# Optimization experiments

Hardware: AMD Instinct MI355X
Metric: run time of the kernel (lower is better)

The kernel has to match this reference:

```python
import jax, jax.numpy as jnp
import numpy as np

B, S, D = 2, 2048, 1024
H, DK, DV = 16, 64, 64


def setup_inputs() -> dict:
    key = jax.random.key(0)
    ks = jax.random.split(key, 9)
    s = 0.02
    return {
        "x": jax.random.normal(ks[0], (B, S, D), dtype=jnp.float32),
        "mask": jnp.zeros((B, S), dtype=bool),  # True = padded position
        "Wq": jax.random.normal(ks[1], (D, H * DK), dtype=jnp.float32) * s,
        "bq": jnp.zeros((H * DK,), dtype=jnp.float32),
        "Wk": jax.random.normal(ks[2], (D, H * DK), dtype=jnp.float32) * s,
        "bk": jnp.zeros((H * DK,), dtype=jnp.float32),
        "Wv": jax.random.normal(ks[3], (D, H * DV), dtype=jnp.float32) * s,
        "bv": jnp.zeros((H * DV,), dtype=jnp.float32),
        "Wo": jax.random.normal(ks[4], (H * DV, D), dtype=jnp.float32) * s,
        "bo": jnp.zeros((D,), dtype=jnp.float32),
    }


def reference(x, mask, Wq, bq, Wk, bk, Wv, bv, Wo, bo):
    Bx, Sx, _ = x.shape
    # projections -> [B, H, S, dk/dv]
    q = (x @ Wq + bq).reshape(Bx, Sx, H, DK).transpose(0, 2, 1, 3)
    k = (x @ Wk + bk).reshape(Bx, Sx, H, DK).transpose(0, 2, 1, 3)
    v = (x @ Wv + bv).reshape(Bx, Sx, H, DV).transpose(0, 2, 1, 3)
    # scaled QK^T: [B, H, Sq, Sk]
    scores = jnp.einsum("bhqd,bhkd->bhqk", q, k) / jnp.sqrt(jnp.float32(DK))
    neg_inf = jnp.float32(-jnp.inf)
    # padding mask: True masks out key positions
    scores = jnp.where(mask[:, None, None, :], neg_inf, scores)
    # causal mask
    causal = jnp.triu(jnp.ones((Sx, Sx), dtype=bool), k=1)
    scores = jnp.where(causal[None, None, :, :], neg_inf, scores)
    attn = jax.nn.softmax(scores, axis=-1)
    out = jnp.einsum("bhqk,bhkd->bhqd", attn, v)  # [B, H, S, dv]
    out = out.transpose(0, 2, 1, 3).reshape(Bx, Sx, H * DV)
    return out @ Wo + bo
```

## Files before the change

kernel.cpp:

```cpp
#include <hip/hip_runtime.h>
#include <stdint.h>

typedef __bf16 bf16_t;
typedef __bf16 bf16x8 __attribute__((ext_vector_type(8)));
typedef float f32x4 __attribute__((ext_vector_type(4)));

#define S_LEN 2048
#define D_MODEL 1024
#define NH 16
#define DKV 64
#define BATCH 2

#define QSCALE 0.1803368801111204f

__device__ __forceinline__ uint16_t f2bfu(float f) {
    union { float f; uint32_t u; } c; c.f = f;
    return (uint16_t)((c.u + 0x7fffu + ((c.u >> 16) & 1u)) >> 16);
}
__device__ __forceinline__ bf16_t f2bf(float f) {
    union { uint16_t s; bf16_t b; } o; o.s = f2bfu(f);
    return o.b;
}
__device__ __forceinline__ uint32_t pack2t(float lo, float hi) {
    union { float f; uint32_t u; } a, b; a.f = lo; b.f = hi;
    return __builtin_amdgcn_perm(b.u, a.u, 0x07060302);
}
__device__ __forceinline__ uint32_t pack2r(float lo, float hi) {
    union { float f; uint32_t u; } a, b; a.f = lo; b.f = hi;
    uint32_t alo = a.u + 0x7fffu + ((a.u >> 16) & 1u);
    uint32_t bhi = b.u + 0x7fffu + ((b.u >> 16) & 1u);
    return __builtin_amdgcn_perm(bhi, alo, 0x07060302);
}
__device__ __forceinline__ float exp2_native(float x) {
    float r;
    asm("v_exp_f32 %0, %1" : "=v"(r) : "v"(x));
    return r;
}
__device__ __forceinline__ void gld_lds16(const bf16_t* g, bf16_t* l) {
    __builtin_amdgcn_global_load_lds(
        (const __attribute__((address_space(1))) void*)g,
        (__attribute__((address_space(3))) void*)l, 16, 0, 0);
}

__global__ __launch_bounds__(256) void k_prep(
    const float* __restrict__ x, bf16_t* __restrict__ xb,
    const float* __restrict__ Wq, const float* __restrict__ Wk,
    const float* __restrict__ Wv, const float* __restrict__ Wo,
    bf16_t* __restrict__ WqkvT, bf16_t* __restrict__ WoT) {
    __shared__ float tile[64][65];
    int bid = blockIdx.x;
    if (bid < 4096) {
        int i = (bid * 256 + threadIdx.x) * 4;
        float4 v = *(const float4*)(x + i);
        xb[i + 0] = f2bf(v.x);
        xb[i + 1] = f2bf(v.y);
        xb[i + 2] = f2bf(v.z);
        xb[i + 3] = f2bf(v.w);
        return;
    }
    int b2 = bid - 4096;
    int k0 = (b2 & 15) * 64;
    int n0 = (b2 >> 4) * 64;
    const float* W; bf16_t* WT; int np, nw;
    if (n0 < 3072) {
        W = (n0 < 1024) ? Wq : (n0 < 2048) ? Wk : Wv;
        np = n0 & 1023; WT = WqkvT; nw = n0;
    } else {
        W = Wo; np = n0 - 3072; WT = WoT; nw = n0 - 3072;
    }
    int tx = threadIdx.x & 63, ty = threadIdx.x >> 6;
    #pragma unroll
    for (int r = ty; r < 64; r += 4)
        tile[r][tx] = W[(size_t)(k0 + r) * 1024 + np + tx];
    __syncthreads();
    #pragma unroll
    for (int r = ty; r < 64; r += 4)
        WT[(size_t)(nw + r) * 1024 + k0 + tx] = f2bf(tile[tx][r]);
}

#define BM 128
#define BN 128
#define BKK 64

__global__ __launch_bounds__(256) void k_gemm_qkv(
    const bf16_t* __restrict__ A, const bf16_t* __restrict__ BT, int K,
    const float* __restrict__ bias0, const float* __restrict__ bias1,
    const float* __restrict__ bias2,
    bf16_t* __restrict__ outQ, bf16_t* __restrict__ outK, bf16_t* __restrict__ outVt) {
    __shared__ __align__(16) bf16_t smem[BM * BKK + BN * BKK];
    bf16_t* const As = smem;
    bf16_t* const Bs = smem + BM * BKK;
    int m0 = blockIdx.x * BM;
    int n0 = blockIdx.y * BN;
    int t = threadIdx.x;
    int wid = t >> 6, lane = t & 63, l15 = lane & 15, quad = lane >> 4;
    int wr = (wid >> 1) * 64, wc = (wid & 1) * 64;
    int srow = t >> 3;
    int schunk = (t & 7) ^ (srow & 7);
    int sldst = (t & 7) * 8;
    const f32x4 fzero = {0.f, 0.f, 0.f, 0.f};
    f32x4 acc[4][4];
    #pragma unroll
    for (int i = 0; i < 4; i++)
        #pragma unroll
        for (int j = 0; j < 4; j++) acc[i][j] = fzero;

    int secb = n0 >> 10;
    int r7 = l15 & 7;
    for (int k0 = 0; k0 < K; k0 += BKK) {
        #pragma unroll
        for (int p = 0; p < 4; p++) {
            int r = p * 32 + srow;
            gld_lds16(&A[(size_t)(m0 + r) * K + k0 + schunk * 8], &As[r * 64 + sldst]);
            gld_lds16(&BT[(size_t)(n0 + r) * K + k0 + schunk * 8], &Bs[r * 64 + sldst]);
        }
        __syncthreads();
        if (secb == 2) {
            #pragma unroll
            for (int kk = 0; kk < BKK; kk += 32) {
                int g = quad + (kk >> 3);
                int col = ((g ^ r7) << 3);
                bf16x8 af[4], bfr[4];
                #pragma unroll
                for (int mt = 0; mt < 4; mt++)
                    af[mt] = *(const bf16x8*)&As[(wr + mt * 16 + l15) * 64 + col];
                #pragma unroll
                for (int nt = 0; nt < 4; nt++)
                    bfr[nt] = *(const bf16x8*)&Bs[(wc + nt * 16 + l15) * 64 + col];
                #pragma unroll
                for (int mt = 0; mt < 4; mt++)
                    #pragma unroll
                    for (int nt = 0; nt < 4; nt++)
                        acc[mt][nt] = __builtin_amdgcn_mfma_f32_16x16x32_bf16(
                            af[mt], bfr[nt], acc[mt][nt], 0, 0, 0);
            }
        } else {
            #pragma unroll
            for (int kk = 0; kk < BKK; kk += 32) {
                int g = quad + (kk >> 3);
                int col = ((g ^ r7) << 3);
                bf16x8 af[4], bfr[4];
                #pragma unroll
                for (int mt = 0; mt < 4; mt++)
                    af[mt] = *(const bf16x8*)&As[(wr + mt * 16 + l15) * 64 + col];
                #pragma unroll
                for (int nt = 0; nt < 4; nt++)
                    bfr[nt] = *(const bf16x8*)&Bs[(wc + nt * 16 + l15) * 64 + col];
                #pragma unroll
                for (int i = 0; i < 4; i++)
                    #pragma unroll
                    for (int j = 0; j < 4; j++)
                        acc[i][j] = __builtin_amdgcn_mfma_f32_16x16x32_bf16(
                            bfr[i], af[j], acc[i][j], 0, 0, 0);
            }
        }
        __syncthreads();
    }

    if (secb == 2) {
        bf16_t* const Ct = smem;
        int nbase = n0 & 1023;
        #pragma unroll
        for (int mt = 0; mt < 4; mt++) {
            #pragma unroll
            for (int nt = 0; nt < 4; nt++) {
                int dl = wc + nt * 16 + l15;
                float bv = bias2[nbase + dl];
                int sl = wr + mt * 16 + quad * 4;
                uint2 pk;
                pk.x = pack2t(acc[mt][nt][0] + bv, acc[mt][nt][1] + bv);
                pk.y = pack2t(acc[mt][nt][2] + bv, acc[mt][nt][3] + bv);
                int c4 = (sl >> 2) ^ ((dl & 7) << 1);
                *(uint2*)&Ct[dl * 128 + c4 * 4] = pk;
            }
        }
        __syncthreads();
        int b = m0 >> 11, sb = m0 & 2047;
        #pragma unroll
        for (int rr = 0; rr < 8; rr++) {
            int row = rr * 16 + (t >> 4);
            int s8 = t & 15;
            int c4 = (s8 * 2) ^ ((row & 7) << 1);
            uint4 vv = *(const uint4*)&Ct[row * 128 + c4 * 4];
            int nn = nbase + row;
            int h = nn >> 6, d = nn & 63;
            *(uint4*)&outVt[(((size_t)(b * NH + h)) * DKV + d) * S_LEN + sb + s8 * 8] = vv;
        }
        return;
    }

    {
        const float* bias = (secb == 0) ? bias0 : bias1;
        bf16_t* outP = (secb == 0) ? outQ : outK;
        float scale = (secb == 0) ? QSCALE : 1.0f;
        #pragma unroll
        for (int i = 0; i < 4; i++) {
            #pragma unroll
            for (int j = 0; j < 4; j++) {
                int nn = (n0 + wc + i * 16 + quad * 4) & 1023;
                float4 bv = *(const float4*)&bias[nn];
                int gr = m0 + wr + j * 16 + l15;
                int b = gr >> 11, s = gr & 2047;
                int h = nn >> 6, d0 = nn & 63;
                float v0 = (acc[i][j][0] + bv.x) * scale;
                float v1 = (acc[i][j][1] + bv.y) * scale;
                float v2 = (acc[i][j][2] + bv.z) * scale;
                float v3 = (acc[i][j][3] + bv.w) * scale;
                uint2 pk;
                pk.x = pack2r(v0, v1);
                pk.y = pack2r(v2, v3);
                *(uint2*)&outP[(((size_t)(b * NH + h)) * S_LEN + s) * DKV + d0] = pk;
            }
        }
    }
}

__global__ __launch_bounds__(256) void k_gemm_out(
    const bf16_t* __restrict__ A, const bf16_t* __restrict__ BT, int N, int K,
    const float* __restrict__ bias, float* __restrict__ outF) {
    __shared__ __align__(16) bf16_t As[128 * 64];
    __shared__ __align__(16) bf16_t Bs[64 * 64];
    int m0 = blockIdx.x * 128;
    int n0 = blockIdx.y * 64;
    int t = threadIdx.x;
    int wid = t >> 6, lane = t & 63, l15 = lane & 15, quad = lane >> 4;
    int wr = wid * 32;
    int srow = t >> 3;
    int schunk = (t & 7) ^ (srow & 7);
    int sldst = (t & 7) * 8;
    const f32x4 fzero = {0.f, 0.f, 0.f, 0.f};
    f32x4 acc[4][2];
    #pragma unroll
    for (int i = 0; i < 4; i++)
        #pragma unroll
        for (int j = 0; j < 2; j++) acc[i][j] = fzero;

    int r7 = l15 & 7;
    for (int k0 = 0; k0 < K; k0 += 64) {
        #pragma unroll
        for (int p = 0; p < 4; p++) {
            int r = p * 32 + srow;
            gld_lds16(&A[(size_t)(m0 + r) * K + k0 + schunk * 8], &As[r * 64 + sldst]);
        }
        #pragma unroll
        for (int p = 0; p < 2; p++) {
            int r = p * 32 + srow;
            gld_lds16(&BT[(size_t)(n0 + r) * K + k0 + schunk * 8], &Bs[r * 64 + sldst]);
        }
        __syncthreads();
        #pragma unroll
        for (int kk = 0; kk < 64; kk += 32) {
            int g = quad + (kk >> 3);
            int col = ((g ^ r7) << 3);
            bf16x8 af[2], bfr[4];
            #pragma unroll
            for (int j = 0; j < 2; j++)
                af[j] = *(const bf16x8*)&As[(wr + j * 16 + l15) * 64 + col];
            #pragma unroll
            for (int i = 0; i < 4; i++)
                bfr[i] = *(const bf16x8*)&Bs[(i * 16 + l15) * 64 + col];
            #pragma unroll
            for (int i = 0; i < 4; i++)
                #pragma unroll
                for (int j = 0; j < 2; j++)
                    acc[i][j] = __builtin_amdgcn_mfma_f32_16x16x32_bf16(
                        bfr[i], af[j], acc[i][j], 0, 0, 0);
        }
        __syncthreads();
    }

    #pragma unroll
    for (int i = 0; i < 4; i++) {
        #pragma unroll
        for (int j = 0; j < 2; j++) {
            int nc = n0 + i * 16 + quad * 4;
            float4 bv = *(const float4*)&bias[nc];
            int mr = m0 + wr + j * 16 + l15;
            float4 o;
            o.x = acc[i][j][0] + bv.x;
            o.y = acc[i][j][1] + bv.y;
            o.z = acc[i][j][2] + bv.z;
            o.w = acc[i][j][3] + bv.w;
            *(float4*)&outF[(size_t)mr * N + nc] = o;
        }
    }
}

__global__ __launch_bounds__(256, 4) void k_attn11(
    const bf16_t* __restrict__ Q, const bf16_t* __restrict__ Kg,
    const bf16_t* __restrict__ Vt, const unsigned char* __restrict__ mask,
    bf16_t* __restrict__ O) {
    __shared__ __align__(16) bf16_t Ks0[64 * 64];
    __shared__ __align__(16) bf16_t Ks1[64 * 64];
    __shared__ __align__(16) bf16_t Vs0[64 * 64];
    __shared__ __align__(16) bf16_t Vs1[64 * 64];
    __shared__ __align__(16) bf16_t Ps[64 * 64];

    int bid = blockIdx.x;
    int bh = bid & 31;
    int u = bid >> 5;
    int a = u & 7, g2 = u >> 3;
    int qt = (g2 == 0) ? 31 - a : (g2 == 1) ? a : (g2 == 2) ? 23 - a : 8 + a;
    int b = bh >> 4, h = bh & 15;
    int t = threadIdx.x;
    int w = t >> 6, lane = t & 63, l15 = lane & 15, quad = lane >> 4;
    int r7 = l15 & 7;

    bool maskany;
    {
        const uint2* mrow = (const uint2*)&mask[b * S_LEN];
        uint2 m0 = mrow[lane], m1 = mrow[lane + 64];
        uint2 m2 = mrow[lane + 128], m3 = mrow[lane + 192];
        uint32_t mo = (m0.x | m0.y) | (m1.x | m1.y) | (m2.x | m2.y) | (m3.x | m3.y);
        maskany = __any(mo != 0);
    }

    const bf16_t* Qrow = Q + ((size_t)bh * S_LEN + qt * 64 + w * 16 + l15) * DKV;
    bf16x8 qf0 = *(const bf16x8*)&Qrow[quad * 8];
    bf16x8 qf1 = *(const bf16x8*)&Qrow[32 + quad * 8];

    const bf16_t* Kbh = Kg + (size_t)bh * S_LEN * DKV;
    const bf16_t* Vbh = Vt + (size_t)bh * DKV * S_LEN;

    const f32x4 fzero = {0.f, 0.f, 0.f, 0.f};
    f32x4 oacc[4];
    f32x4 lacc = fzero;
    #pragma unroll
    for (int nt = 0; nt < 4; nt++) oacc[nt] = fzero;

    const bf16_t one_b = (bf16_t)1.0f;
    const bf16x8 onesf = {one_b, one_b, one_b, one_b, one_b, one_b, one_b, one_b};

    int qg = qt * 64 + w * 16 + l15;

    int sr = t >> 3;
    int sc = (t & 7) ^ (sr & 7);
    int sl = (t & 7) * 8;

    #pragma unroll
    for (int p = 0; p < 2; p++) {
        int r = p * 32 + sr;
        gld_lds16(&Kbh[(size_t)r * DKV + sc * 8], &Ks0[r * 64 + sl]);
        gld_lds16(&Vbh[(size_t)r * S_LEN + sc * 8], &Vs0[r * 64 + sl]);
    }
    __syncthreads();

    auto TILE = [&](const bf16_t* __restrict__ Kr, const bf16_t* __restrict__ Vr,
                    bf16_t* __restrict__ Kw, bf16_t* __restrict__ Vw, int kt) {
        if (kt < qt) {
            int kb2 = (kt + 1) * 64;
            #pragma unroll
            for (int p = 0; p < 2; p++) {
                int r = p * 32 + sr;
                gld_lds16(&Kbh[(size_t)(kb2 + r) * DKV + sc * 8], &Kw[r * 64 + sl]);
                gld_lds16(&Vbh[(size_t)r * S_LEN + kb2 + sc * 8], &Vw[r * 64 + sl]);
            }
        }
        int kbase = kt * 64;

        f32x4 sacc[4];
        #pragma unroll
        for (int mt = 0; mt < 4; mt++) sacc[mt] = fzero;
        #pragma unroll
        for (int kk = 0; kk < 64; kk += 32) {
            bf16x8 qf = kk ? qf1 : qf0;
            int col = (((quad + (kk >> 3)) ^ r7) << 3);
            bf16x8 af[4];
            #pragma unroll
            for (int mt = 0; mt < 4; mt++)
                af[mt] = *(const bf16x8*)&Kr[(mt * 16 + l15) * 64 + col];
            __builtin_amdgcn_s_setprio(1);
            #pragma unroll
            for (int mt = 0; mt < 4; mt++)
                sacc[mt] = __builtin_amdgcn_mfma_f32_16x16x32_bf16(af[mt], qf, sacc[mt], 0, 0, 0);
            __builtin_amdgcn_s_setprio(0);
        }

        if (maskany) {
            #pragma unroll
            for (int mt = 0; mt < 4; mt++) {
                uint32_t mb = *(const uint32_t*)&mask[b * S_LEN + kbase + mt * 16 + quad * 4];
                #pragma unroll
                for (int r = 0; r < 4; r++)
                    sacc[mt][r] += (float)((mb >> (8 * r)) & 0xffu) * -1e30f;
            }
        }
        if (kt == qt) {
            #pragma unroll
            for (int mt = 0; mt < 4; mt++) {
                int kgb = kbase + mt * 16 + quad * 4;
                #pragma unroll
                for (int r = 0; r < 4; r++)
                    if (kgb + r > qg) sacc[mt][r] = -1e30f;
            }
        }
        #pragma unroll
        for (int mt = 0; mt < 4; mt++) {
            uint2 pk;
            pk.x = pack2t(exp2_native(sacc[mt][0]), exp2_native(sacc[mt][1]));
            pk.y = pack2t(exp2_native(sacc[mt][2]), exp2_native(sacc[mt][3]));
            int pc = (mt * 2 + (quad >> 1)) ^ r7;
            *(uint2*)&Ps[(w * 16 + l15) * 64 + pc * 8 + (quad & 1) * 4] = pk;
        }

        #pragma unroll
        for (int kk = 0; kk < 64; kk += 32) {
            bf16x8 pf = *(const bf16x8*)&Ps[(w * 16 + l15) * 64 +
                                             (((quad + (kk >> 3)) ^ r7) << 3)];
            int vcol = (((quad + (kk >> 3)) ^ r7) << 3);
            bf16x8 vf[4];
            #pragma unroll
            for (int nt = 0; nt < 4; nt++)
                vf[nt] = *(const bf16x8*)&Vr[(nt * 16 + l15) * 64 + vcol];
            __builtin_amdgcn_s_setprio(1);
            #pragma unroll
            for (int nt = 0; nt < 4; nt++)
                oacc[nt] = __builtin_amdgcn_mfma_f32_16x16x32_bf16(pf, vf[nt], oacc[nt], 0, 0, 0);
            lacc = __builtin_amdgcn_mfma_f32_16x16x32_bf16(pf, onesf, lacc, 0, 0, 0);
            __builtin_amdgcn_s_setprio(0);
        }

        if (kt < qt) __syncthreads();
    };

    for (int kt = 0; kt <= qt; kt += 2) {
        TILE(Ks0, Vs0, Ks1, Vs1, kt);
        if (kt + 1 <= qt) TILE(Ks1, Vs1, Ks0, Vs0, kt + 1);
    }

    #pragma unroll
    for (int r = 0; r < 4; r++) {
        float l = lacc[r];
        float invl = l > 0.f ? 1.f / l : 0.f;
        int q = qt * 64 + w * 16 + quad * 4 + r;
        #pragma unroll
        for (int nt = 0; nt < 4; nt++) {
            int d = nt * 16 + l15;
            O[((size_t)b * S_LEN + q) * D_MODEL + h * DKV + d] = f2bf(oacc[nt][r] * invl);
        }
    }
}

extern "C" void kernel_launch(void* const* d_in, const int* in_sizes, int n_in,
                              void* d_out, int out_size, void* d_ws, size_t ws_size,
                              hipStream_t stream) {
    const float* x = (const float*)d_in[0];
    const unsigned char* mask = (const unsigned char*)d_in[1];
    const float* Wq = (const float*)d_in[2];
    const float* bq = (const float*)d_in[3];
    const float* Wk = (const float*)d_in[4];
    const float* bk = (const float*)d_in[5];
    const float* Wv = (const float*)d_in[6];
    const float* bv = (const float*)d_in[7];
    const float* Wo = (const float*)d_in[8];
    const float* bo = (const float*)d_in[9];
    float* out = (float*)d_out;

    char* ws = (char*)d_ws;
    const size_t MB = 1024 * 1024;
    bf16_t* xb    = (bf16_t*)(ws + 0 * MB);
    bf16_t* WqkvT = (bf16_t*)(ws + 8 * MB);
    bf16_t* WoT   = (bf16_t*)(ws + 14 * MB);
    bf16_t* Qb    = (bf16_t*)(ws + 16 * MB);
    bf16_t* Kb    = (bf16_t*)(ws + 24 * MB);
    bf16_t* Vtb   = (bf16_t*)(ws + 32 * MB);
    bf16_t* AOb   = (bf16_t*)(ws + 40 * MB);

    k_prep<<<dim3(4096 + 1024), dim3(256), 0, stream>>>(
        x, xb, Wq, Wk, Wv, Wo, WqkvT, WoT);
    k_gemm_qkv<<<dim3(32, 24), dim3(256), 0, stream>>>(
        xb, WqkvT, 1024, bq, bk, bv, Qb, Kb, Vtb);
    k_attn11<<<dim3(1024), dim3(256), 0, stream>>>(Qb, Kb, Vtb, mask, AOb);
    k_gemm_out<<<dim3(32, 16), dim3(256), 0, stream>>>(
        AOb, WoT, 1024, 1024, bo, out);
}
```

Measured before the change: 181.3 us.

## Double query tile per block to reuse K/V tiles across two row groups

After: 194.3 us. 7.2% more time.

```diff
diff --git a/kernel.cpp b/kernel.cpp
--- a/kernel.cpp
+++ b/kernel.cpp
@@ -286,7 +286,7 @@
     }
 }
 
-__global__ __launch_bounds__(256, 4) void k_attn11(
+__global__ __launch_bounds__(256, 2) void k_attn12(
     const bf16_t* __restrict__ Q, const bf16_t* __restrict__ Kg,
     const bf16_t* __restrict__ Vt, const unsigned char* __restrict__ mask,
     bf16_t* __restrict__ O) {
@@ -294,13 +294,12 @@
     __shared__ __align__(16) bf16_t Ks1[64 * 64];
     __shared__ __align__(16) bf16_t Vs0[64 * 64];
     __shared__ __align__(16) bf16_t Vs1[64 * 64];
-    __shared__ __align__(16) bf16_t Ps[64 * 64];
+    __shared__ __align__(16) bf16_t Ps[128 * 64];
 
     int bid = blockIdx.x;
     int bh = bid & 31;
     int u = bid >> 5;
-    int a = u & 7, g2 = u >> 3;
-    int qt = (g2 == 0) ? 31 - a : (g2 == 1) ? a : (g2 == 2) ? 23 - a : 8 + a;
+    int qt = (u < 8) ? (15 - u) : (u - 8);
     int b = bh >> 4, h = bh & 15;
     int t = threadIdx.x;
     int w = t >> 6, lane = t & 63, l15 = lane & 15, quad = lane >> 4;
@@ -315,23 +314,28 @@
         maskany = __any(mo != 0);
     }
 
-    const bf16_t* Qrow = Q + ((size_t)bh * S_LEN + qt * 64 + w * 16 + l15) * DKV;
-    bf16x8 qf0 = *(const bf16x8*)&Qrow[quad * 8];
-    bf16x8 qf1 = *(const bf16x8*)&Qrow[32 + quad * 8];
+    const bf16_t* Q0 = Q + ((size_t)bh * S_LEN + qt * 128 + w * 32 + l15) * DKV;
+    bf16x8 qf[2][2];
+    qf[0][0] = *(const bf16x8*)&Q0[quad * 8];
+    qf[0][1] = *(const bf16x8*)&Q0[32 + quad * 8];
+    qf[1][0] = *(const bf16x8*)&Q0[16 * DKV + quad * 8];
+    qf[1][1] = *(const bf16x8*)&Q0[16 * DKV + 32 + quad * 8];
 
     const bf16_t* Kbh = Kg + (size_t)bh * S_LEN * DKV;
     const bf16_t* Vbh = Vt + (size_t)bh * DKV * S_LEN;
 
     const f32x4 fzero = {0.f, 0.f, 0.f, 0.f};
-    f32x4 oacc[4];
-    f32x4 lacc = fzero;
-    #pragma unroll
-    for (int nt = 0; nt < 4; nt++) oacc[nt] = fzero;
+    f32x4 oacc[2][4];
+    f32x4 lacc[2] = {fzero, fzero};
+    #pragma unroll
+    for (int g = 0; g < 2; g++)
+        #pragma unroll
+        for (int nt = 0; nt < 4; nt++) oacc[g][nt] = fzero;
 
     const bf16_t one_b = (bf16_t)1.0f;
     const bf16x8 onesf = {one_b, one_b, one_b, one_b, one_b, one_b, one_b, one_b};
 
-    int qg = qt * 64 + w * 16 + l15;
+    int qmin0 = qt * 128 + w * 32;
 
     int sr = t >> 3;
     int sc = (t & 7) ^ (sr & 7);
@@ -345,9 +349,11 @@
     }
     __syncthreads();
 
+    int ktmax = 2 * qt + 1;
+
     auto TILE = [&](const bf16_t* __restrict__ Kr, const bf16_t* __restrict__ Vr,
                     bf16_t* __restrict__ Kw, bf16_t* __restrict__ Vw, int kt) {
-        if (kt < qt) {
+        if (kt < ktmax) {
             int kb2 = (kt + 1) * 64;
             #pragma unroll
             for (int p = 0; p < 2; p++) {
@@ -357,86 +363,124 @@
             }
         }
         int kbase = kt * 64;
-
-        f32x4 sacc[4];
-        #pragma unroll
-        for (int mt = 0; mt < 4; mt++) sacc[mt] = fzero;
-        #pragma unroll
-        for (int kk = 0; kk < 64; kk += 32) {
-            bf16x8 qf = kk ? qf1 : qf0;
-            int col = (((quad + (kk >> 3)) ^ r7) << 3);
-            bf16x8 af[4];
-            #pragma unroll
-            for (int mt = 0; mt < 4; mt++)
-                af[mt] = *(const bf16x8*)&Kr[(mt * 16 + l15) * 64 + col];
-            __builtin_amdgcn_s_setprio(1);
-            #pragma unroll
-            for (int mt = 0; mt < 4; mt++)
-                sacc[mt] = __builtin_amdgcn_mfma_f32_16x16x32_bf16(af[mt], qf, sacc[mt], 0, 0, 0);
-            __builtin_amdgcn_s_setprio(0);
-        }
-
-        if (maskany) {
-            #pragma unroll
-            for (int mt = 0; mt < 4; mt++) {
-                uint32_t mb = *(const uint32_t*)&mask[b * S_LEN + kbase + mt * 16 + quad * 4];
-                #pragma unroll
-                for (int r = 0; r < 4; r++)
-                    sacc[mt][r] += (float)((mb >> (8 * r)) & 0xffu) * -1e30f;
-            }
-        }
-        if (kt == qt) {
-            #pragma unroll
-            for (int mt = 0; mt < 4; mt++) {
-                int kgb = kbase + mt * 16 + quad * 4;
-                #pragma unroll
-                for (int r = 0; r < 4; r++)
-                    if (kgb + r > qg) sacc[mt][r] = -1e30f;
-            }
-        }
-        #pragma unroll
-        for (int mt = 0; mt < 4; mt++) {
-            uint2 pk;
-            pk.x = pack2t(exp2_native(sacc[mt][0]), exp2_native(sacc[mt][1]));
-            pk.y = pack2t(exp2_native(sacc[mt][2]), exp2_native(sacc[mt][3]));
-            int pc = (mt * 2 + (quad >> 1)) ^ r7;
-            *(uint2*)&Ps[(w * 16 + l15) * 64 + pc * 8 + (quad & 1) * 4] = pk;
-        }
-
-        #pragma unroll
-        for (int kk = 0; kk < 64; kk += 32) {
-            bf16x8 pf = *(const bf16x8*)&Ps[(w * 16 + l15) * 64 +
-                                             (((quad + (kk >> 3)) ^ r7) << 3)];
-            int vcol = (((quad + (kk >> 3)) ^ r7) << 3);
-            bf16x8 vf[4];
-            #pragma unroll
-            for (int nt = 0; nt < 4; nt++)
-                vf[nt] = *(const bf16x8*)&Vr[(nt * 16 + l15) * 64 + vcol];
-            __builtin_amdgcn_s_setprio(1);
-            #pragma unroll
-            for (int nt = 0; nt < 4; nt++)
-                oacc[nt] = __builtin_amdgcn_mfma_f32_16x16x32_bf16(pf, vf[nt], oacc[nt], 0, 0, 0);
-            lacc = __builtin_amdgcn_mfma_f32_16x16x32_bf16(pf, onesf, lacc, 0, 0, 0);
-            __builtin_amdgcn_s_setprio(0);
-        }
-
-        if (kt < qt) __syncthreads();
+        bool act0 = (kbase <= qmin0 + 15);
+        bool act1 = (kbase <= qmin0 + 31);
+
+        if (act1) {
+            f32x4 sacc[2][4];
+            #pragma unroll
+            for (int g = 0; g < 2; g++)
+                #pragma unroll
+                for (int mt = 0; mt < 4; mt++) sacc[g][mt] = fzero;
+
+            #pragma unroll
+            for (int kk = 0; kk < 64; kk += 32) {
+                int col = (((quad + (kk >> 3)) ^ r7) << 3);
+                bf16x8 af[4];
+                #pragma unroll
+                for (int mt = 0; mt < 4; mt++)
+                    af[mt] = *(const bf16x8*)&Kr[(mt * 16 + l15) * 64 + col];
+                __builtin_amdgcn_s_setprio(1);
+                if (act0) {
+                    #pragma unroll
+                    for (int mt = 0; mt < 4; mt++)
+                        sacc[0][mt] = __builtin_amdgcn_mfma_f32_16x16x32_bf16(
+                            af[mt], qf[0][kk ? 1 : 0], sacc[0][mt], 0, 0, 0);
+                }
+                #pragma unroll
+                for (int mt = 0; mt < 4; mt++)
+                    sacc[1][mt] = __builtin_amdgcn_mfma_f32_16x16x32_bf16(
+                        af[mt], qf[1][kk ? 1 : 0], sacc[1][mt], 0, 0, 0);
+                __builtin_amdgcn_s_setprio(0);
+            }
+
+            if (maskany) {
+                #pragma unroll
+                for (int mt = 0; mt < 4; mt++) {
+                    uint32_t mb = *(const uint32_t*)&mask[b * S_LEN + kbase + mt * 16 + quad * 4];
+                    #pragma unroll
+                    for (int r = 0; r < 4; r++) {
+                        float pen = (float)((mb >> (8 * r)) & 0xffu) * -1e30f;
+                        sacc[0][mt][r] += pen;
+                        sacc[1][mt][r] += pen;
+                    }
+                }
+            }
+            #pragma unroll
+            for (int g = 0; g < 2; g++) {
+                int qming = qmin0 + 16 * g;
+                if (kbase + 63 > qming) {
+                    int qg = qming + l15;
+                    #pragma unroll
+                    for (int mt = 0; mt < 4; mt++) {
+                        int kgb = kbase + mt * 16 + quad * 4;
+                        #pragma unroll
+                        for (int r = 0; r < 4; r++)
+                            if (kgb + r > qg) sacc[g][mt][r] = -1e30f;
+                    }
+                }
+            }
+            #pragma unroll
+            for (int g = 0; g < 2; g++) {
+                if (g == 0 && !act0) continue;
+                int prow = (w * 32 + g * 16 + l15) * 64;
+                #pragma unroll
+                for (int mt = 0; mt < 4; mt++) {
+                    uint2 pk;
+                    pk.x = pack2t(exp2_native(sacc[g][mt][0]), exp2_native(sacc[g][mt][1]));
+                    pk.y = pack2t(exp2_native(sacc[g][mt][2]), exp2_native(sacc[g][mt][3]));
+                    int pc = (mt * 2 + (quad >> 1)) ^ r7;
+                    *(uint2*)&Ps[prow + pc * 8 + (quad & 1) * 4] = pk;
+                }
+            }
+
+            #pragma unroll
+            for (int kk = 0; kk < 64; kk += 32) {
+                int vcol = (((quad + (kk >> 3)) ^ r7) << 3);
+                bf16x8 vf[4];
+                #pragma unroll
+                for (int nt = 0; nt < 4; nt++)
+                    vf[nt] = *(const bf16x8*)&Vr[(nt * 16 + l15) * 64 + vcol];
+                bf16x8 pf0, pf1;
+                if (act0) pf0 = *(const bf16x8*)&Ps[(w * 32 + l15) * 64 + vcol];
+                pf1 = *(const bf16x8*)&Ps[(w * 32 + 16 + l15) * 64 + vcol];
+                __builtin_amdgcn_s_setprio(1);
+                if (act0) {
+                    #pragma unroll
+                    for (int nt = 0; nt < 4; nt++)
+                        oacc[0][nt] = __builtin_amdgcn_mfma_f32_16x16x32_bf16(
+                            pf0, vf[nt], oacc[0][nt], 0, 0, 0);
+                    lacc[0] = __builtin_amdgcn_mfma_f32_16x16x32_bf16(pf0, onesf, lacc[0], 0, 0, 0);
+                }
+                #pragma unroll
+                for (int nt = 0; nt < 4; nt++)
+                    oacc[1][nt] = __builtin_amdgcn_mfma_f32_16x16x32_bf16(
+                        pf1, vf[nt], oacc[1][nt], 0, 0, 0);
+                lacc[1] = __builtin_amdgcn_mfma_f32_16x16x32_bf16(pf1, onesf, lacc[1], 0, 0, 0);
+                __builtin_amdgcn_s_setprio(0);
+            }
+        }
+
+        if (kt < ktmax) __syncthreads();
     };
 
-    for (int kt = 0; kt <= qt; kt += 2) {
+    for (int kt = 0; kt <= ktmax; kt += 2) {
         TILE(Ks0, Vs0, Ks1, Vs1, kt);
-        if (kt + 1 <= qt) TILE(Ks1, Vs1, Ks0, Vs0, kt + 1);
-    }
-
-    #pragma unroll
-    for (int r = 0; r < 4; r++) {
-        float l = lacc[r];
-        float invl = l > 0.f ? 1.f / l : 0.f;
-        int q = qt * 64 + w * 16 + quad * 4 + r;
-        #pragma unroll
-        for (int nt = 0; nt < 4; nt++) {
-            int d = nt * 16 + l15;
-            O[((size_t)b * S_LEN + q) * D_MODEL + h * DKV + d] = f2bf(oacc[nt][r] * invl);
+        TILE(Ks1, Vs1, Ks0, Vs0, kt + 1);
+    }
+
+    #pragma unroll
+    for (int g = 0; g < 2; g++) {
+        #pragma unroll
+        for (int r = 0; r < 4; r++) {
+            float l = lacc[g][r];
+            float invl = l > 0.f ? 1.f / l : 0.f;
+            int q = qt * 128 + w * 32 + g * 16 + quad * 4 + r;
+            #pragma unroll
+            for (int nt = 0; nt < 4; nt++) {
+                int d = nt * 16 + l15;
+                O[((size_t)b * S_LEN + q) * D_MODEL + h * DKV + d] = f2bf(oacc[g][nt][r] * invl);
+            }
         }
     }
 }
@@ -470,7 +514,7 @@
         x, xb, Wq, Wk, Wv, Wo, WqkvT, WoT);
     k_gemm_qkv<<<dim3(32, 24), dim3(256), 0, stream>>>(
         xb, WqkvT, 1024, bq, bk, bv, Qb, Kb, Vtb);
-    k_attn11<<<dim3(1024), dim3(256), 0, stream>>>(Qb, Kb, Vtb, mask, AOb);
+    k_attn12<<<dim3(512), dim3(256), 0, stream>>>(Qb, Kb, Vtb, mask, AOb);
     k_gemm_out<<<dim3(32, 16), dim3(256), 0, stream>>>(
         AOb, WoT, 1024, 1024, bo, out);
 }
```

## Double-buffer QKV GEMM LDS tiles with BK=32 and prefetch next stage

Applied to the files above, without the earlier changes.

Result: no change. 179.9 us (-0.8%).

```diff
diff --git a/kernel.cpp b/kernel.cpp
--- a/kernel.cpp
+++ b/kernel.cpp
@@ -80,24 +80,25 @@
 
 #define BM 128
 #define BN 128
-#define BKK 64
 
 __global__ __launch_bounds__(256) void k_gemm_qkv(
     const bf16_t* __restrict__ A, const bf16_t* __restrict__ BT, int K,
     const float* __restrict__ bias0, const float* __restrict__ bias1,
     const float* __restrict__ bias2,
     bf16_t* __restrict__ outQ, bf16_t* __restrict__ outK, bf16_t* __restrict__ outVt) {
-    __shared__ __align__(16) bf16_t smem[BM * BKK + BN * BKK];
-    bf16_t* const As = smem;
-    bf16_t* const Bs = smem + BM * BKK;
+    __shared__ __align__(16) bf16_t smem[4 * 128 * 32];
+    bf16_t* const As0 = smem;
+    bf16_t* const As1 = smem + 128 * 32;
+    bf16_t* const Bs0 = smem + 2 * 128 * 32;
+    bf16_t* const Bs1 = smem + 3 * 128 * 32;
     int m0 = blockIdx.x * BM;
     int n0 = blockIdx.y * BN;
     int t = threadIdx.x;
     int wid = t >> 6, lane = t & 63, l15 = lane & 15, quad = lane >> 4;
     int wr = (wid >> 1) * 64, wc = (wid & 1) * 64;
-    int srow = t >> 3;
-    int schunk = (t & 7) ^ (srow & 7);
-    int sldst = (t & 7) * 8;
+    int sr = t >> 2;
+    int sc = (t & 3) ^ (sr & 3);
+    int sl = (t & 3) * 8;
     const f32x4 fzero = {0.f, 0.f, 0.f, 0.f};
     f32x4 acc[4][4];
     #pragma unroll
@@ -106,58 +107,57 @@
         for (int j = 0; j < 4; j++) acc[i][j] = fzero;
 
     int secb = n0 >> 10;
-    int r7 = l15 & 7;
-    for (int k0 = 0; k0 < K; k0 += BKK) {
-        #pragma unroll
-        for (int p = 0; p < 4; p++) {
-            int r = p * 32 + srow;
-            gld_lds16(&A[(size_t)(m0 + r) * K + k0 + schunk * 8], &As[r * 64 + sldst]);
-            gld_lds16(&BT[(size_t)(n0 + r) * K + k0 + schunk * 8], &Bs[r * 64 + sldst]);
-        }
-        __syncthreads();
+    int r3 = l15 & 3;
+    int colA = (quad ^ r3) << 3;
+
+    auto STAGE = [&](bf16_t* __restrict__ Ad, bf16_t* __restrict__ Bd, int k0) {
+        #pragma unroll
+        for (int p = 0; p < 2; p++) {
+            int r = p * 64 + sr;
+            gld_lds16(&A[(size_t)(m0 + r) * K + k0 + sc * 8], &Ad[r * 32 + sl]);
+            gld_lds16(&BT[(size_t)(n0 + r) * K + k0 + sc * 8], &Bd[r * 32 + sl]);
+        }
+    };
+
+    auto STEP = [&](const bf16_t* __restrict__ Ar, const bf16_t* __restrict__ Br,
+                    bf16_t* __restrict__ Aw, bf16_t* __restrict__ Bw, int i) {
+        if (i + 1 < 32) STAGE(Aw, Bw, (i + 1) * 32);
+        bf16x8 af[4], bfr[4];
+        #pragma unroll
+        for (int mt = 0; mt < 4; mt++)
+            af[mt] = *(const bf16x8*)&Ar[(wr + mt * 16 + l15) * 32 + colA];
+        #pragma unroll
+        for (int nt = 0; nt < 4; nt++)
+            bfr[nt] = *(const bf16x8*)&Br[(wc + nt * 16 + l15) * 32 + colA];
+        __builtin_amdgcn_s_setprio(1);
         if (secb == 2) {
             #pragma unroll
-            for (int kk = 0; kk < BKK; kk += 32) {
-                int g = quad + (kk >> 3);
-                int col = ((g ^ r7) << 3);
-                bf16x8 af[4], bfr[4];
-                #pragma unroll
-                for (int mt = 0; mt < 4; mt++)
-                    af[mt] = *(const bf16x8*)&As[(wr + mt * 16 + l15) * 64 + col];
+            for (int mt = 0; mt < 4; mt++)
                 #pragma unroll
                 for (int nt = 0; nt < 4; nt++)
-                    bfr[nt] = *(const bf16x8*)&Bs[(wc + nt * 16 + l15) * 64 + col];
+                    acc[mt][nt] = __builtin_amdgcn_mfma_f32_16x16x32_bf16(
+                        af[mt], bfr[nt], acc[mt][nt], 0, 0, 0);
+        } else {
+            #pragma unroll
+            for (int i2 = 0; i2 < 4; i2++)
                 #pragma unroll
-                for (int mt = 0; mt < 4; mt++)
-                    #pragma unroll
-                    for (int nt = 0; nt < 4; nt++)
-                        acc[mt][nt] = __builtin_amdgcn_mfma_f32_16x16x32_bf16(
-                            af[mt], bfr[nt], acc[mt][nt], 0, 0, 0);
-            }
-        } else {
-            #pragma unroll
-            for (int kk = 0; kk < BKK; kk += 32) {
-                int g = quad + (kk >> 3);
-                int col = ((g ^ r7) << 3);
-                bf16x8 af[4], bfr[4];
-                #pragma unroll
-                for (int mt = 0; mt < 4; mt++)
-                    af[mt] = *(const bf16x8*)&As[(wr + mt * 16 + l15) * 64 + col];
-                #pragma unroll
-                for (int nt = 0; nt < 4; nt++)
-                    bfr[nt] = *(const bf16x8*)&Bs[(wc + nt * 16 + l15) * 64 + col];
-                #pragma unroll
-                for (int i = 0; i < 4; i++)
-                    #pragma unroll
-                    for (int j = 0; j < 4; j++)
-                        acc[i][j] = __builtin_amdgcn_mfma_f32_16x16x32_bf16(
-                            bfr[i], af[j], acc[i][j], 0, 0, 0);
-            }
-        }
+                for (int j = 0; j < 4; j++)
+                    acc[i2][j] = __builtin_amdgcn_mfma_f32_16x16x32_bf16(
+                        bfr[i2], af[j], acc[i2][j], 0, 0, 0);
+        }
+        __builtin_amdgcn_s_setprio(0);
+        if (i + 1 < 32) __syncthreads();
+    };
+
+    STAGE(As0, Bs0, 0);
+    __syncthreads();
+    for (int i = 0; i < 32; i += 2) {
+        STEP(As0, Bs0, As1, Bs1, i);
+        STEP(As1, Bs1, As0, Bs0, i + 1);
+    }
+
+    if (secb == 2) {
         __syncthreads();
-    }
-
-    if (secb == 2) {
         bf16_t* const Ct = smem;
         int nbase = n0 & 1023;
         #pragma unroll
@@ -166,11 +166,11 @@
             for (int nt = 0; nt < 4; nt++) {
                 int dl = wc + nt * 16 + l15;
                 float bv = bias2[nbase + dl];
-                int sl = wr + mt * 16 + quad * 4;
+                int sl2 = wr + mt * 16 + quad * 4;
                 uint2 pk;
                 pk.x = pack2t(acc[mt][nt][0] + bv, acc[mt][nt][1] + bv);
                 pk.y = pack2t(acc[mt][nt][2] + bv, acc[mt][nt][3] + bv);
-                int c4 = (sl >> 2) ^ ((dl & 7) << 1);
+                int c4 = (sl2 >> 2) ^ ((dl & 7) << 1);
                 *(uint2*)&Ct[dl * 128 + c4 * 4] = pk;
             }
         }
@@ -332,6 +332,7 @@
     const bf16x8 onesf = {one_b, one_b, one_b, one_b, one_b, one_b, one_b, one_b};
 
     int qg = qt * 64 + w * 16 + l15;
+    int qmin = qt * 64 + w * 16;
 
     int sr = t >> 3;
     int sc = (t & 7) ^ (sr & 7);
@@ -405,9 +406,8 @@
 
         #pragma unroll
         for (int kk = 0; kk < 64; kk += 32) {
-            bf16x8 pf = *(const bf16x8*)&Ps[(w * 16 + l15) * 64 +
-                                             (((quad + (kk >> 3)) ^ r7) << 3)];
             int vcol = (((quad + (kk >> 3)) ^ r7) << 3);
+            bf16x8 pf = *(const bf16x8*)&Ps[(w * 16 + l15) * 64 + vcol];
             bf16x8 vf[4];
             #pragma unroll
             for (int nt = 0; nt < 4; nt++)
```
